# Kernel tuning notes

Measured on AMD Instinct MI355X. Metric: run time of the kernel, lower is better.

Reference implementation:

```python
import jax, jax.numpy as jnp
import numpy as np

B, H, W, C = 8, 64, 64, 256
NUM_HEADS = 8
HEAD_DIM = C // NUM_HEADS
H_SP, W_SP = 64, 8  # idx=0: h_sp=H, w_sp=split_size[1]
SCALE = HEAD_DIM ** -0.5


def img2windows(img):
    # img: [B, C, H, W] -> [B*nW, h_sp*w_sp, C]
    b, c, h, w = img.shape
    x = img.reshape(b, c, h // H_SP, H_SP, w // W_SP, W_SP)
    x = jnp.transpose(x, (0, 2, 4, 3, 5, 1))
    return x.reshape(-1, H_SP * W_SP, c)


def im2cswin(x):
    # x: [B, L, C] -> [B*nW, heads, h_sp*w_sp, head_dim]
    xi = jnp.transpose(x, (0, 2, 1)).reshape(B, C, H, W)
    xw = img2windows(xi)
    xw = xw.reshape(-1, H_SP * W_SP, NUM_HEADS, HEAD_DIM)
    return jnp.transpose(xw, (0, 2, 1, 3))


def get_lepe(x, conv_w, conv_b):
    xi = jnp.transpose(x, (0, 2, 1)).reshape(B, C, H, W)
    xi = xi.reshape(B, C, H // H_SP, H_SP, W // W_SP, W_SP)
    xi = jnp.transpose(xi, (0, 2, 4, 1, 3, 5)).reshape(-1, C, H_SP, W_SP)
    # depthwise 3x3 conv, padding 1
    lepe = jax.lax.conv_general_dilated(
        xi, conv_w, window_strides=(1, 1), padding=((1, 1), (1, 1)),
        feature_group_count=C, dimension_numbers=('NCHW', 'OIHW', 'NCHW'))
    lepe = lepe + conv_b[None, :, None, None]
    def to_heads(t):
        t = t.reshape(-1, NUM_HEADS, HEAD_DIM, H_SP * W_SP)
        return jnp.transpose(t, (0, 1, 3, 2))
    return to_heads(xi), to_heads(lepe)


def windows2img(xw):
    # xw: [B*nW, h_sp*w_sp, C] -> [B, H, W, C]
    x = xw.reshape(B, H // H_SP, W // W_SP, H_SP, W_SP, C)
    x = jnp.transpose(x, (0, 1, 3, 2, 4, 5))
    return x.reshape(B, H, W, C)


def setup_inputs() -> dict:
    key = jax.random.key(0)
    k1, k2, k3 = jax.random.split(key, 3)
    x = jax.random.normal(k1, (3, B, H * W, C), dtype=jnp.float32)
    conv_w = jax.random.normal(k2, (C, 1, 3, 3), dtype=jnp.float32) * 0.1
    conv_b = jax.random.normal(k3, (C,), dtype=jnp.float32) * 0.1
    return {"x": x, "conv_w": conv_w, "conv_b": conv_b}


def reference(x, conv_w, conv_b):
    q, k, v = x[0], x[1], x[2]
    qh = im2cswin(q) * SCALE          # [nW*B, h, S, d]
    kh = im2cswin(k)
    vh, lepe = get_lepe(v, conv_w, conv_b)
    attn = jnp.einsum('whsd,whtd->whst', qh, kh)
    attn = jax.nn.softmax(attn, axis=-1)
    out = jnp.einsum('whst,whtd->whsd', attn, vh) + lepe
    out = jnp.transpose(out, (0, 2, 1, 3)).reshape(-1, H_SP * W_SP, C)
    return windows2img(out).reshape(B, H * W, C)
```

## Files before the change

kernel.cpp:

```cpp
#include <hip/hip_runtime.h>

typedef __attribute__((ext_vector_type(8))) __bf16 bf16x8;
typedef __attribute__((ext_vector_type(4))) __bf16 bf16x4;
typedef __attribute__((ext_vector_type(4))) _Float16 half4;
typedef __attribute__((ext_vector_type(4))) float floatx4;

static __device__ __forceinline__ floatx4 mfma_qk(bf16x8 a, bf16x8 b, floatx4 c) {
    return __builtin_amdgcn_mfma_f32_16x16x32_bf16(a, b, c, 0, 0, 0);
}
static __device__ __forceinline__ floatx4 mfma_pv(half4 a, half4 b, floatx4 c) {
    return __builtin_amdgcn_mfma_f32_16x16x16f16(a, b, c, 0, 0, 0);
}

#define QSCALE 0.25504099302278787f

__global__ __launch_bounds__(256, 2) void lepe_attn_kernel(
    const float* __restrict__ x, const float* __restrict__ conv_w,
    const float* __restrict__ conv_b, float* __restrict__ out)
{
    const int bx = blockIdx.x;
    const int wi = bx >> 3, hd = bx & 7;
    const int b = wi >> 3, wblk = wi & 7;
    const int tid = threadIdx.x;
    const int wave = tid >> 6, lane = tid & 63;
    const int g = lane >> 4, ln = lane & 15;

    __shared__ __align__(16) __bf16   Ks[512][32];
    __shared__ __align__(16) _Float16 VsT[32][522];
    __shared__ float Wc[32][9];
    __shared__ float Bc[32];

    const float* qp = x;
    const float* kp = x + 8 * 4096 * 256;
    const float* vp = x + 2 * 8 * 4096 * 256;
    const int base  = b * 4096 * 256;
    const int cbase = hd * 32;
    const int wcol0 = wblk * 8;

    for (int i = tid; i < 4096; i += 256) {
        int t = i >> 3, f = i & 7;
        int l = ((t >> 3) << 6) + wcol0 + (t & 7);
        int off = base + l * 256 + cbase + f * 4;
        float4 k4 = *(const float4*)(kp + off);
        bf16x4 kk = { (__bf16)k4.x, (__bf16)k4.y, (__bf16)k4.z, (__bf16)k4.w };
        *(bf16x4*)&Ks[t][f * 4] = kk;
        float4 v4 = *(const float4*)(vp + off);
        VsT[f*4+0][t] = (_Float16)v4.x;
        VsT[f*4+1][t] = (_Float16)v4.y;
        VsT[f*4+2][t] = (_Float16)v4.z;
        VsT[f*4+3][t] = (_Float16)v4.w;
    }
    for (int i = tid; i < 288; i += 256)
        Wc[i / 9][i % 9] = conv_w[(cbase + i / 9) * 9 + (i % 9)];
    if (tid < 32) Bc[tid] = conv_b[cbase + tid];
    __syncthreads();

    for (int qc = wave; qc < 16; qc += 4) {
        bf16x8 bq0, bq1;
        {
            int s = qc * 32 + ln;
            int l = ((s >> 3) << 6) + wcol0 + (s & 7);
            const float* qb = qp + base + l * 256 + cbase + g * 8;
            float4 a = *(const float4*)qb, c = *(const float4*)(qb + 4);
            bq0[0] = (__bf16)(a.x * QSCALE); bq0[1] = (__bf16)(a.y * QSCALE);
            bq0[2] = (__bf16)(a.z * QSCALE); bq0[3] = (__bf16)(a.w * QSCALE);
            bq0[4] = (__bf16)(c.x * QSCALE); bq0[5] = (__bf16)(c.y * QSCALE);
            bq0[6] = (__bf16)(c.z * QSCALE); bq0[7] = (__bf16)(c.w * QSCALE);
            s = qc * 32 + 16 + ln;
            l = ((s >> 3) << 6) + wcol0 + (s & 7);
            qb = qp + base + l * 256 + cbase + g * 8;
            a = *(const float4*)qb; c = *(const float4*)(qb + 4);
            bq1[0] = (__bf16)(a.x * QSCALE); bq1[1] = (__bf16)(a.y * QSCALE);
            bq1[2] = (__bf16)(a.z * QSCALE); bq1[3] = (__bf16)(a.w * QSCALE);
            bq1[4] = (__bf16)(c.x * QSCALE); bq1[5] = (__bf16)(c.y * QSCALE);
            bq1[6] = (__bf16)(c.z * QSCALE); bq1[7] = (__bf16)(c.w * QSCALE);
        }

        floatx4 aLo0 = {0.f,0.f,0.f,0.f}, aHi0 = {0.f,0.f,0.f,0.f};
        floatx4 aLo1 = {0.f,0.f,0.f,0.f}, aHi1 = {0.f,0.f,0.f,0.f};
        float lsum0 = 0.f, lsum1 = 0.f;
        const floatx4 zf = {0.f,0.f,0.f,0.f};

        #pragma unroll 4
        for (int tb = 0; tb < 32; tb++) {
            bf16x8 ak = *(const bf16x8*)&Ks[tb * 16 + ln][g * 8];
            floatx4 sc0 = mfma_qk(ak, bq0, zf);
            floatx4 sc1 = mfma_qk(ak, bq1, zf);

            half4 ph0, ph1;
            #pragma unroll
            for (int r = 0; r < 4; r++) {
                float p0 = __builtin_amdgcn_exp2f(sc0[r]);
                lsum0 += p0; ph0[r] = (_Float16)p0;
                float p1 = __builtin_amdgcn_exp2f(sc1[r]);
                lsum1 += p1; ph1[r] = (_Float16)p1;
            }

            int tcol = tb * 16 + g * 4;
            const unsigned* r0 = (const unsigned*)&VsT[ln][0];
            const unsigned* r1 = (const unsigned*)&VsT[16 + ln][0];
            half4 av0, av1;
            ((unsigned*)&av0)[0] = r0[tcol >> 1];
            ((unsigned*)&av0)[1] = r0[(tcol >> 1) + 1];
            ((unsigned*)&av1)[0] = r1[tcol >> 1];
            ((unsigned*)&av1)[1] = r1[(tcol >> 1) + 1];

            aLo0 = mfma_pv(av0, ph0, aLo0);
            aHi0 = mfma_pv(av1, ph0, aHi0);
            aLo1 = mfma_pv(av0, ph1, aLo1);
            aHi1 = mfma_pv(av1, ph1, aHi1);
        }

        lsum0 += __shfl_xor(lsum0, 16); lsum0 += __shfl_xor(lsum0, 32);
        lsum1 += __shfl_xor(lsum1, 16); lsum1 += __shfl_xor(lsum1, 32);
        float inv0 = 1.0f / lsum0, inv1 = 1.0f / lsum1;

        #pragma unroll
        for (int ss = 0; ss < 2; ss++) {
            int s = qc * 32 + ss * 16 + ln;
            int h = s >> 3, w = s & 7;
            int l = h * 64 + wcol0 + w;
            float inv = ss ? inv1 : inv0;
            floatx4 alo = ss ? aLo1 : aLo0;
            floatx4 ahi = ss ? aHi1 : aHi0;
            float4 olo, ohi;
            #pragma unroll
            for (int r = 0; r < 4; r++) {
                int ddl = g * 4 + r;
                float lepl = Bc[ddl];
                float leph = Bc[16 + ddl];
                #pragma unroll
                for (int ky = 0; ky < 3; ky++) {
                    int hh = h + ky - 1;
                    bool okh = (hh >= 0) & (hh < 64);
                    #pragma unroll
                    for (int kx = 0; kx < 3; kx++) {
                        int ww = w + kx - 1;
                        bool ok = okh & (ww >= 0) & (ww < 8);
                        float vl = ok ? (float)VsT[ddl][hh * 8 + ww] : 0.f;
                        float vh = ok ? (float)VsT[16 + ddl][hh * 8 + ww] : 0.f;
                        lepl = fmaf(vl, Wc[ddl][ky * 3 + kx], lepl);
                        leph = fmaf(vh, Wc[16 + ddl][ky * 3 + kx], leph);
                    }
                }
                ((float*)&olo)[r] = alo[r] * inv + lepl;
                ((float*)&ohi)[r] = ahi[r] * inv + leph;
            }
            float* ob = out + base + l * 256 + cbase;
            *(float4*)(ob + g * 4) = olo;
            *(float4*)(ob + 16 + g * 4) = ohi;
        }
    }
}

extern "C" void kernel_launch(void* const* d_in, const int* in_sizes, int n_in,
                              void* d_out, int out_size, void* d_ws, size_t ws_size,
                              hipStream_t stream) {
    const float* x  = (const float*)d_in[0];
    const float* cw = (const float*)d_in[1];
    const float* cb = (const float*)d_in[2];
    float* out = (float*)d_out;
    lepe_attn_kernel<<<dim3(512), dim3(256), 0, stream>>>(x, cw, cb, out);
}
```

Measured before the change: 186.1 us.

## Split query rows across two blocks and pipeline K/V loads with compute

The grid doubles so each block handles half the query rows of a window-head, and each wave keeps four query tiles in registers to reuse each K fragment. K is double-buffered in 128-key chunks, and V is appended incrementally, with the next chunk's global loads issued before computing on the current one. This aims to overlap global load latency with MFMA work and raise parallelism. In exchange, each window's K/V is loaded twice (once per half-block), register pressure rises, and a barrier is added per chunk.

```diff
diff --git a/kernel.cpp b/kernel.cpp
--- a/kernel.cpp
+++ b/kernel.cpp
@@ -19,13 +19,15 @@
     const float* __restrict__ conv_b, float* __restrict__ out)
 {
     const int bx = blockIdx.x;
-    const int wi = bx >> 3, hd = bx & 7;
+    const int wi = bx >> 4;
+    const int hd = (bx >> 1) & 7;
+    const int shalf = bx & 1;
     const int b = wi >> 3, wblk = wi & 7;
     const int tid = threadIdx.x;
     const int wave = tid >> 6, lane = tid & 63;
     const int g = lane >> 4, ln = lane & 15;
 
-    __shared__ __align__(16) __bf16   Ks[512][32];
+    __shared__ __align__(16) __bf16   Ks[2][128][32];
     __shared__ __align__(16) _Float16 VsT[32][522];
     __shared__ float Wc[32][9];
     __shared__ float Bc[32];
@@ -36,14 +38,35 @@
     const int base  = b * 4096 * 256;
     const int cbase = hd * 32;
     const int wcol0 = wblk * 8;
-
-    for (int i = tid; i < 4096; i += 256) {
+    const int qcb   = shalf * 8 + wave;
+
+    bf16x8 bq[4];
+    #pragma unroll
+    for (int c = 0; c < 2; c++) {
+        #pragma unroll
+        for (int ss = 0; ss < 2; ss++) {
+            int s = (qcb + 4 * c) * 32 + ss * 16 + ln;
+            int l = ((s >> 3) << 6) + wcol0 + (s & 7);
+            const float* qb = qp + base + l * 256 + cbase + g * 8;
+            float4 a = *(const float4*)qb, d = *(const float4*)(qb + 4);
+            bf16x8 q;
+            q[0] = (__bf16)(a.x * QSCALE); q[1] = (__bf16)(a.y * QSCALE);
+            q[2] = (__bf16)(a.z * QSCALE); q[3] = (__bf16)(a.w * QSCALE);
+            q[4] = (__bf16)(d.x * QSCALE); q[5] = (__bf16)(d.y * QSCALE);
+            q[6] = (__bf16)(d.z * QSCALE); q[7] = (__bf16)(d.w * QSCALE);
+            bq[c * 2 + ss] = q;
+        }
+    }
+
+    #pragma unroll
+    for (int p = 0; p < 4; p++) {
+        int i = tid + p * 256;
         int t = i >> 3, f = i & 7;
         int l = ((t >> 3) << 6) + wcol0 + (t & 7);
         int off = base + l * 256 + cbase + f * 4;
         float4 k4 = *(const float4*)(kp + off);
         bf16x4 kk = { (__bf16)k4.x, (__bf16)k4.y, (__bf16)k4.z, (__bf16)k4.w };
-        *(bf16x4*)&Ks[t][f * 4] = kk;
+        *(bf16x4*)&Ks[0][t][f * 4] = kk;
         float4 v4 = *(const float4*)(vp + off);
         VsT[f*4+0][t] = (_Float16)v4.x;
         VsT[f*4+1][t] = (_Float16)v4.y;
@@ -55,48 +78,38 @@
     if (tid < 32) Bc[tid] = conv_b[cbase + tid];
     __syncthreads();
 
-    for (int qc = wave; qc < 16; qc += 4) {
-        bf16x8 bq0, bq1;
-        {
-            int s = qc * 32 + ln;
-            int l = ((s >> 3) << 6) + wcol0 + (s & 7);
-            const float* qb = qp + base + l * 256 + cbase + g * 8;
-            float4 a = *(const float4*)qb, c = *(const float4*)(qb + 4);
-            bq0[0] = (__bf16)(a.x * QSCALE); bq0[1] = (__bf16)(a.y * QSCALE);
-            bq0[2] = (__bf16)(a.z * QSCALE); bq0[3] = (__bf16)(a.w * QSCALE);
-            bq0[4] = (__bf16)(c.x * QSCALE); bq0[5] = (__bf16)(c.y * QSCALE);
-            bq0[6] = (__bf16)(c.z * QSCALE); bq0[7] = (__bf16)(c.w * QSCALE);
-            s = qc * 32 + 16 + ln;
-            l = ((s >> 3) << 6) + wcol0 + (s & 7);
-            qb = qp + base + l * 256 + cbase + g * 8;
-            a = *(const float4*)qb; c = *(const float4*)(qb + 4);
-            bq1[0] = (__bf16)(a.x * QSCALE); bq1[1] = (__bf16)(a.y * QSCALE);
-            bq1[2] = (__bf16)(a.z * QSCALE); bq1[3] = (__bf16)(a.w * QSCALE);
-            bq1[4] = (__bf16)(c.x * QSCALE); bq1[5] = (__bf16)(c.y * QSCALE);
-            bq1[6] = (__bf16)(c.z * QSCALE); bq1[7] = (__bf16)(c.w * QSCALE);
-        }
-
-        floatx4 aLo0 = {0.f,0.f,0.f,0.f}, aHi0 = {0.f,0.f,0.f,0.f};
-        floatx4 aLo1 = {0.f,0.f,0.f,0.f}, aHi1 = {0.f,0.f,0.f,0.f};
-        float lsum0 = 0.f, lsum1 = 0.f;
-        const floatx4 zf = {0.f,0.f,0.f,0.f};
-
+    floatx4 aLo[4], aHi[4];
+    float lsum[4];
+    #pragma unroll
+    for (int u = 0; u < 4; u++) {
+        aLo[u] = (floatx4){0.f,0.f,0.f,0.f};
+        aHi[u] = (floatx4){0.f,0.f,0.f,0.f};
+        lsum[u] = 0.f;
+    }
+    const floatx4 zf = {0.f,0.f,0.f,0.f};
+
+    for (int j = 0; j < 4; j++) {
+        float4 kx[4], vx[4];
+        int tloc[4], floc[4];
+        if (j < 3) {
+            #pragma unroll
+            for (int p = 0; p < 4; p++) {
+                int i = tid + p * 256;
+                int t = i >> 3, f = i & 7;
+                tloc[p] = t; floc[p] = f;
+                int tg = 128 * (j + 1) + t;
+                int l = ((tg >> 3) << 6) + wcol0 + (tg & 7);
+                int off = base + l * 256 + cbase + f * 4;
+                kx[p] = *(const float4*)(kp + off);
+                vx[p] = *(const float4*)(vp + off);
+            }
+        }
+
+        const __bf16 (*KT)[32] = Ks[j & 1];
         #pragma unroll 4
-        for (int tb = 0; tb < 32; tb++) {
-            bf16x8 ak = *(const bf16x8*)&Ks[tb * 16 + ln][g * 8];
-            floatx4 sc0 = mfma_qk(ak, bq0, zf);
-            floatx4 sc1 = mfma_qk(ak, bq1, zf);
-
-            half4 ph0, ph1;
-            #pragma unroll
-            for (int r = 0; r < 4; r++) {
-                float p0 = __builtin_amdgcn_exp2f(sc0[r]);
-                lsum0 += p0; ph0[r] = (_Float16)p0;
-                float p1 = __builtin_amdgcn_exp2f(sc1[r]);
-                lsum1 += p1; ph1[r] = (_Float16)p1;
-            }
-
-            int tcol = tb * 16 + g * 4;
+        for (int tl = 0; tl < 8; tl++) {
+            bf16x8 ak = *(const bf16x8*)&KT[tl * 16 + ln][g * 8];
+            int tcol = j * 128 + tl * 16 + g * 4;
             const unsigned* r0 = (const unsigned*)&VsT[ln][0];
             const unsigned* r1 = (const unsigned*)&VsT[16 + ln][0];
             half4 av0, av1;
@@ -104,25 +117,55 @@
             ((unsigned*)&av0)[1] = r0[(tcol >> 1) + 1];
             ((unsigned*)&av1)[0] = r1[tcol >> 1];
             ((unsigned*)&av1)[1] = r1[(tcol >> 1) + 1];
-
-            aLo0 = mfma_pv(av0, ph0, aLo0);
-            aHi0 = mfma_pv(av1, ph0, aHi0);
-            aLo1 = mfma_pv(av0, ph1, aLo1);
-            aHi1 = mfma_pv(av1, ph1, aHi1);
-        }
-
-        lsum0 += __shfl_xor(lsum0, 16); lsum0 += __shfl_xor(lsum0, 32);
-        lsum1 += __shfl_xor(lsum1, 16); lsum1 += __shfl_xor(lsum1, 32);
-        float inv0 = 1.0f / lsum0, inv1 = 1.0f / lsum1;
-
+            #pragma unroll
+            for (int u = 0; u < 4; u++) {
+                floatx4 sc = mfma_qk(ak, bq[u], zf);
+                half4 ph;
+                #pragma unroll
+                for (int r = 0; r < 4; r++) {
+                    float pp = __builtin_amdgcn_exp2f(sc[r]);
+                    lsum[u] += pp;
+                    ph[r] = (_Float16)pp;
+                }
+                aLo[u] = mfma_pv(av0, ph, aLo[u]);
+                aHi[u] = mfma_pv(av1, ph, aHi[u]);
+            }
+        }
+
+        if (j < 3) {
+            #pragma unroll
+            for (int p = 0; p < 4; p++) {
+                int t = tloc[p], f = floc[p];
+                bf16x4 kk = { (__bf16)kx[p].x, (__bf16)kx[p].y,
+                              (__bf16)kx[p].z, (__bf16)kx[p].w };
+                *(bf16x4*)&Ks[(j + 1) & 1][t][f * 4] = kk;
+                int tg = 128 * (j + 1) + t;
+                VsT[f*4+0][tg] = (_Float16)vx[p].x;
+                VsT[f*4+1][tg] = (_Float16)vx[p].y;
+                VsT[f*4+2][tg] = (_Float16)vx[p].z;
+                VsT[f*4+3][tg] = (_Float16)vx[p].w;
+            }
+        }
+        __syncthreads();
+    }
+
+    float inv[4];
+    #pragma unroll
+    for (int u = 0; u < 4; u++) {
+        float t = lsum[u];
+        t += __shfl_xor(t, 16); t += __shfl_xor(t, 32);
+        inv[u] = 1.0f / t;
+    }
+
+    #pragma unroll
+    for (int c = 0; c < 2; c++) {
         #pragma unroll
         for (int ss = 0; ss < 2; ss++) {
-            int s = qc * 32 + ss * 16 + ln;
+            int u = c * 2 + ss;
+            int s = (qcb + 4 * c) * 32 + ss * 16 + ln;
             int h = s >> 3, w = s & 7;
             int l = h * 64 + wcol0 + w;
-            float inv = ss ? inv1 : inv0;
-            floatx4 alo = ss ? aLo1 : aLo0;
-            floatx4 ahi = ss ? aHi1 : aHi0;
+            floatx4 alo = aLo[u], ahi = aHi[u];
             float4 olo, ohi;
             #pragma unroll
             for (int r = 0; r < 4; r++) {
@@ -134,17 +177,17 @@
                     int hh = h + ky - 1;
                     bool okh = (hh >= 0) & (hh < 64);
                     #pragma unroll
-                    for (int kx = 0; kx < 3; kx++) {
-                        int ww = w + kx - 1;
+                    for (int kx2 = 0; kx2 < 3; kx2++) {
+                        int ww = w + kx2 - 1;
                         bool ok = okh & (ww >= 0) & (ww < 8);
                         float vl = ok ? (float)VsT[ddl][hh * 8 + ww] : 0.f;
                         float vh = ok ? (float)VsT[16 + ddl][hh * 8 + ww] : 0.f;
-                        lepl = fmaf(vl, Wc[ddl][ky * 3 + kx], lepl);
-                        leph = fmaf(vh, Wc[16 + ddl][ky * 3 + kx], leph);
+                        lepl = fmaf(vl, Wc[ddl][ky * 3 + kx2], lepl);
+                        leph = fmaf(vh, Wc[16 + ddl][ky * 3 + kx2], leph);
                     }
                 }
-                ((float*)&olo)[r] = alo[r] * inv + lepl;
-                ((float*)&ohi)[r] = ahi[r] * inv + leph;
+                ((float*)&olo)[r] = alo[r] * inv[u] + lepl;
+                ((float*)&ohi)[r] = ahi[r] * inv[u] + leph;
             }
             float* ob = out + base + l * 256 + cbase;
             *(float4*)(ob + g * 4) = olo;
@@ -160,5 +203,5 @@
     const float* cw = (const float*)d_in[1];
     const float* cb = (const float*)d_in[2];
     float* out = (float*)d_out;
-    lepe_attn_kernel<<<dim3(512), dim3(256), 0, stream>>>(x, cw, cb, out);
-}
+    lepe_attn_kernel<<<dim3(1024), dim3(256), 0, stream>>>(x, cw, cb, out);
+}
```

New measurement: 191.8 us. 3.0% more time.
